# Optimization experiments

Measured on AMD Instinct MI355X. Metric: run time of the kernel, lower is better.

## Reference

```python
import jax, jax.numpy as jnp
import numpy as np

BETA = 0.01
NUM_EMBEDDINGS = 8192
EMBEDDING_DIM = 512


def setup_inputs() -> dict:
    key = jax.random.key(0)
    k1, k2 = jax.random.split(key)
    inputs = jax.random.normal(k1, (16, 2048, EMBEDDING_DIM), dtype=jnp.float32)
    # nn.Embedding weight init: uniform(-1/K, 1/K)
    lim = 1.0 / NUM_EMBEDDINGS
    codebook = jax.random.uniform(k2, (NUM_EMBEDDINGS, EMBEDDING_DIM),
                                  dtype=jnp.float32, minval=-lim, maxval=lim)
    return {"inputs": inputs, "codebook": codebook}


def reference(inputs, codebook):
    D = codebook.shape[1]
    x = inputs.reshape(-1, D)  # [N, D]
    distances = (jnp.sum(x * x, axis=1, keepdims=True)
                 + jnp.sum(codebook * codebook, axis=1)
                 - 2.0 * jnp.einsum('nd,kd->nk', x, codebook))
    encoding_indices = jnp.argmin(distances, axis=1)  # [N]
    quantized = codebook[encoding_indices].reshape(inputs.shape)
    sg = jax.lax.stop_gradient
    mse = lambda a, b: jnp.mean((a - b) ** 2)
    commitment_loss = mse(sg(quantized), inputs) + BETA * mse(quantized, sg(inputs))
    # straight-through estimator
    quantized_st = inputs + sg(quantized - inputs)
    return quantized_st, commitment_loss, encoding_indices
```

## Files before the change

kernel.cpp:

```cpp
#include <hip/hip_runtime.h>
#include <hip/hip_bf16.h>
#include <hip/hip_fp16.h>

typedef unsigned short ushortT;
typedef _Float16 half8 __attribute__((ext_vector_type(8)));
typedef float f32x4 __attribute__((ext_vector_type(4)));

#define N_ROWS   32768
#define DIM      512
#define K_CODES  8192
#define BETA     0.01f

#define LOSS_OFF 16777216
#define IDX_OFF  16777217

#define SC_XH_F      0
#define SC_EH_F      8388608
#define SC_GCODE_F   10485760
#define SC_GCNT_F    11010048
#define SC_FIXMIN_F  11042816
#define SC_FIXLIST_F 11108352

#define WS_XX_OFF     0
#define WS_IDX_OFF    32768
#define WS_PART_OFF   65536
#define WS_CNT_OFF    73728

#define FLT_BIG 3.402823466e+38f
#define W_ACC   0.08192f
#define GCAP    16

typedef __attribute__((address_space(1))) const unsigned int GUI;
typedef __attribute__((address_space(3))) unsigned int LUI;
__device__ __forceinline__ void gload16(const void* g, void* l) {
    __builtin_amdgcn_global_load_lds((GUI*)g, (LUI*)l, 16, 0, 0);
}

__global__ __launch_bounds__(256) void vq_prep(const float* __restrict__ x,
                                               const float* __restrict__ cb,
                                               ushortT* __restrict__ xh,
                                               ushortT* __restrict__ eh) {
    const size_t gid = (size_t)blockIdx.x * 256 + threadIdx.x;
    const size_t off8 = gid * 8;
    const float* src;
    ushortT* dst;
    float sc;
    if (off8 < 16777216UL) { src = x + off8; dst = xh + off8; sc = 1.0f; }
    else { size_t o = off8 - 16777216UL; src = cb + o; dst = eh + o; sc = 1024.0f; }
    float4 v0 = *reinterpret_cast<const float4*>(src);
    float4 v1 = *reinterpret_cast<const float4*>(src + 4);
    union { ushortT s[8]; uint4 v; } u;
    u.s[0] = __half_as_ushort(__float2half(v0.x * sc));
    u.s[1] = __half_as_ushort(__float2half(v0.y * sc));
    u.s[2] = __half_as_ushort(__float2half(v0.z * sc));
    u.s[3] = __half_as_ushort(__float2half(v0.w * sc));
    u.s[4] = __half_as_ushort(__float2half(v1.x * sc));
    u.s[5] = __half_as_ushort(__float2half(v1.y * sc));
    u.s[6] = __half_as_ushort(__float2half(v1.z * sc));
    u.s[7] = __half_as_ushort(__float2half(v1.w * sc));
    *reinterpret_cast<uint4*>(dst) = u.v;
}

__global__ __launch_bounds__(256) void vq_xx_kernel(const float* __restrict__ x,
                                                    float* __restrict__ xx) {
    __shared__ float l[4][512];
    const int wave = threadIdx.x >> 6;
    const int lane = threadIdx.x & 63;
    const int row = blockIdx.x * 4 + wave;
    const float* xr = x + (size_t)row * DIM;
#pragma unroll
    for (int i = 0; i < 2; ++i) {
        float4 v = *reinterpret_cast<const float4*>(xr + lane * 8 + i * 4);
        float4 q = make_float4(v.x * v.x, v.y * v.y, v.z * v.z, v.w * v.w);
        *reinterpret_cast<float4*>(&l[wave][lane * 8 + i * 4]) = q;
    }
    __syncthreads();
    if (lane == 0) {
        float B[4];
#pragma unroll
        for (int q = 0; q < 4; ++q) {
            const float* a = &l[wave][q * 128];
            float r0 = a[0], r1 = a[1], r2 = a[2], r3 = a[3];
            float r4 = a[4], r5 = a[5], r6 = a[6], r7 = a[7];
            for (int i = 8; i < 128; i += 8) {
                r0 += a[i + 0]; r1 += a[i + 1]; r2 += a[i + 2]; r3 += a[i + 3];
                r4 += a[i + 4]; r5 += a[i + 5]; r6 += a[i + 6]; r7 += a[i + 7];
            }
            B[q] = ((r0 + r1) + (r2 + r3)) + ((r4 + r5) + (r6 + r7));
        }
        xx[row] = (B[0] + B[1]) + (B[2] + B[3]);
    }
}

#define BM 128
#define BN 128
#define BKH 64
#define KHALF 4096
#define NSTEP 256
#define ABUF 8192

__global__ __launch_bounds__(512, 4) void vq_margmin(
    const ushortT* __restrict__ xh, const ushortT* __restrict__ eh,
    unsigned* __restrict__ gCode, unsigned* __restrict__ gCnt,
    int* __restrict__ fixcnt, int* __restrict__ fixlist) {
    __shared__ ushortT As[2][ABUF];
    __shared__ ushortT Bs[2][ABUF];
    float* v1L        = (float*)&As[0][0];
    float* rowThr     = (float*)&As[0][512];
    unsigned* candCnt = (unsigned*)&As[0][768];
    int* flagL        = (int*)&As[0][1024];
    ushortT* candList = &As[0][1280];

    const int t = threadIdx.x;
    const int l = t & 63;
    const int wid = t >> 6;
    const int wm = wid >> 1;
    const int wn = wid & 1;
    const int lr = l & 15;
    const int lg = l >> 4;
    const int rowBase = (blockIdx.x >> 1) * BM;
    const int kbase = (blockIdx.x & 1) * KHALF;

    const ushortT* aSrc0; const ushortT* aSrc1;
    const ushortT* bSrc0; const ushortT* bSrc1;
    int dOff0, dOff1;
    {
        int f0 = t, r0 = f0 >> 3, g0 = f0 & 7, gs0 = g0 ^ (r0 & 7);
        int f1 = t + 512, r1 = f1 >> 3, g1 = f1 & 7, gs1 = g1 ^ (r1 & 7);
        aSrc0 = xh + (size_t)(rowBase + r0) * DIM + gs0 * 8;
        aSrc1 = xh + (size_t)(rowBase + r1) * DIM + gs1 * 8;
        bSrc0 = eh + (size_t)(kbase + r0) * DIM + gs0 * 8;
        bSrc1 = eh + (size_t)(kbase + r1) * DIM + gs1 * 8;
        dOff0 = f0 * 8; dOff1 = f1 * 8;
    }
    int offA[2][2], offB[4][2];
#pragma unroll
    for (int kk = 0; kk < 2; ++kk) {
#pragma unroll
        for (int mf = 0; mf < 2; ++mf) {
            int row = wm * 32 + mf * 16 + lr;
            int pg = (kk * 4 + lg) ^ (row & 7);
            offA[mf][kk] = row * 128 + pg * 16;
        }
#pragma unroll
        for (int nf = 0; nf < 4; ++nf) {
            int col = wn * 64 + nf * 16 + lr;
            int pg = (kk * 4 + lg) ^ (col & 7);
            offB[nf][kk] = col * 128 + pg * 16;
        }
    }

    float v1[2][4], v2m[2][4], v3m[2][4];
    int i1[2][4], i2[2][4];
#pragma unroll
    for (int mf = 0; mf < 2; ++mf)
#pragma unroll
        for (int rr = 0; rr < 4; ++rr) {
            v1[mf][rr] = -FLT_BIG; v2m[mf][rr] = -FLT_BIG; v3m[mf][rr] = -FLT_BIG;
            i1[mf][rr] = 0; i2[mf][rr] = 0;
        }

    f32x4 acc[2][4];

#define STAGE(stp, b) do {                                                     \
    int kt_ = ((stp) & 7) * BKH;                                               \
    size_t bAdd_ = (size_t)((stp) >> 3) * BN * DIM + kt_;                      \
    gload16(aSrc0 + kt_, &As[b][dOff0]);                                       \
    gload16(aSrc1 + kt_, &As[b][dOff1]);                                       \
    gload16(bSrc0 + bAdd_, &Bs[b][dOff0]);                                     \
    gload16(bSrc1 + bAdd_, &Bs[b][dOff1]);                                     \
} while (0)

#define COMPUTE(CUR) do {                                                      \
    _Pragma("unroll")                                                          \
    for (int kk = 0; kk < 2; ++kk) {                                           \
        half8 a0 = *reinterpret_cast<const half8*>((const char*)&As[CUR][0] + offA[0][kk]); \
        half8 a1 = *reinterpret_cast<const half8*>((const char*)&As[CUR][0] + offA[1][kk]); \
        half8 b0 = *reinterpret_cast<const half8*>((const char*)&Bs[CUR][0] + offB[0][kk]); \
        half8 b1 = *reinterpret_cast<const half8*>((const char*)&Bs[CUR][0] + offB[1][kk]); \
        half8 b2 = *reinterpret_cast<const half8*>((const char*)&Bs[CUR][0] + offB[2][kk]); \
        half8 b3 = *reinterpret_cast<const half8*>((const char*)&Bs[CUR][0] + offB[3][kk]); \
        acc[0][0] = __builtin_amdgcn_mfma_f32_16x16x32_f16(a0, b0, acc[0][0], 0, 0, 0); \
        acc[0][1] = __builtin_amdgcn_mfma_f32_16x16x32_f16(a0, b1, acc[0][1], 0, 0, 0); \
        acc[0][2] = __builtin_amdgcn_mfma_f32_16x16x32_f16(a0, b2, acc[0][2], 0, 0, 0); \
        acc[0][3] = __builtin_amdgcn_mfma_f32_16x16x32_f16(a0, b3, acc[0][3], 0, 0, 0); \
        acc[1][0] = __builtin_amdgcn_mfma_f32_16x16x32_f16(a1, b0, acc[1][0], 0, 0, 0); \
        acc[1][1] = __builtin_amdgcn_mfma_f32_16x16x32_f16(a1, b1, acc[1][1], 0, 0, 0); \
        acc[1][2] = __builtin_amdgcn_mfma_f32_16x16x32_f16(a1, b2, acc[1][2], 0, 0, 0); \
        acc[1][3] = __builtin_amdgcn_mfma_f32_16x16x32_f16(a1, b3, acc[1][3], 0, 0, 0); \
    }                                                                          \
} while (0)

#define EPILOGUE(k0t_) do {                                                    \
    _Pragma("unroll")                                                          \
    for (int mf = 0; mf < 2; ++mf) {                                           \
        _Pragma("unroll")                                                      \
        for (int nf = 0; nf < 4; ++nf) {                                       \
            const int tag = ((k0t_) << 2) | nf;                                \
            _Pragma("unroll")                                                  \
            for (int rr = 0; rr < 4; ++rr) {                                   \
                float s = acc[mf][nf][rr];                                     \
                bool g1 = s > v1[mf][rr];                                      \
                bool g2 = s > v2m[mf][rr];                                     \
                bool g3 = s > v3m[mf][rr];                                     \
                v3m[mf][rr] = g2 ? v2m[mf][rr] : (g3 ? s : v3m[mf][rr]);       \
                i2[mf][rr]  = g1 ? i1[mf][rr]  : (g2 ? tag : i2[mf][rr]);      \
                v2m[mf][rr] = g1 ? v1[mf][rr]  : (g2 ? s : v2m[mf][rr]);       \
                i1[mf][rr]  = g1 ? tag : i1[mf][rr];                           \
                v1[mf][rr]  = g1 ? s   : v1[mf][rr];                           \
            }                                                                  \
        }                                                                      \
    }                                                                          \
} while (0)

    STAGE(0, 0);
    for (int sp = 0; sp < NSTEP; sp += 2) {
        if ((sp & 7) == 0) {
#pragma unroll
            for (int mf = 0; mf < 2; ++mf)
#pragma unroll
                for (int nf = 0; nf < 4; ++nf)
                    acc[mf][nf] = (f32x4){0.f, 0.f, 0.f, 0.f};
        }
        STAGE(sp + 1, 1);
        asm volatile("s_waitcnt vmcnt(4)" ::: "memory");
        __builtin_amdgcn_sched_barrier(0);
        __builtin_amdgcn_s_barrier();
        COMPUTE(0);
        __builtin_amdgcn_s_barrier();
        if (sp + 2 < NSTEP) {
            STAGE(sp + 2, 0);
            asm volatile("s_waitcnt vmcnt(4)" ::: "memory");
        } else {
            asm volatile("s_waitcnt vmcnt(0)" ::: "memory");
        }
        __builtin_amdgcn_sched_barrier(0);
        __builtin_amdgcn_s_barrier();
        COMPUTE(1);
        if ((sp & 7) == 6) EPILOGUE(sp >> 3);
        __builtin_amdgcn_s_barrier();
    }

    __syncthreads();
#pragma unroll
    for (int mf = 0; mf < 2; ++mf)
#pragma unroll
        for (int rr = 0; rr < 4; ++rr) {
            float v = v1[mf][rr];
            v = fmaxf(v, __shfl_xor(v, 1));
            v = fmaxf(v, __shfl_xor(v, 2));
            v = fmaxf(v, __shfl_xor(v, 4));
            v = fmaxf(v, __shfl_xor(v, 8));
            if (lr == 0) v1L[(wm * 32 + mf * 16 + lg * 4 + rr) * 2 + wn] = v;
        }
    __syncthreads();
    if (t < BM) {
        rowThr[t] = fmaxf(v1L[t * 2], v1L[t * 2 + 1]) - W_ACC;
        candCnt[t] = 0u;
        flagL[t] = 0;
    }
    __syncthreads();
#pragma unroll
    for (int mf = 0; mf < 2; ++mf)
#pragma unroll
        for (int rr = 0; rr < 4; ++rr) {
            const int row = wm * 32 + mf * 16 + lg * 4 + rr;
            const float thr = rowThr[row];
            if (v1[mf][rr] >= thr) {
                unsigned pos = atomicAdd(&candCnt[row], 1u);
                int tg = i1[mf][rr];
                int code = kbase + ((tg >> 2) << 7) + (wn << 6) + ((tg & 3) << 4) + lr;
                if (pos < GCAP) candList[row * GCAP + pos] = (ushortT)code;
                else flagL[row] = 1;
            }
            if (v2m[mf][rr] >= thr) {
                unsigned pos = atomicAdd(&candCnt[row], 1u);
                int tg = i2[mf][rr];
                int code = kbase + ((tg >> 2) << 7) + (wn << 6) + ((tg & 3) << 4) + lr;
                if (pos < GCAP) candList[row * GCAP + pos] = (ushortT)code;
                else flagL[row] = 1;
            }
            if (v3m[mf][rr] >= thr) flagL[row] = 1;
        }
    __syncthreads();
    if (t < BM) {
        const int grow = rowBase + t;
        unsigned cc = candCnt[t];
        bool ovf = (flagL[t] != 0) || (cc > GCAP);
        if (!ovf) {
            for (unsigned j = 0; j < cc; ++j) {
                unsigned pos = atomicAdd(&gCnt[grow], 1u);
                if (pos < GCAP) gCode[(size_t)grow * GCAP + pos] = candList[t * GCAP + j];
                else ovf = true;
            }
        }
        if (ovf) {
            int p = atomicAdd(fixcnt, 1);
            fixlist[p] = grow;
        }
    }
#undef STAGE
#undef COMPUTE
#undef EPILOGUE
}

__global__ __launch_bounds__(256) void vq_refine(
    const float* __restrict__ x, const float* __restrict__ cb,
    const float* __restrict__ xx, const unsigned* __restrict__ gCode,
    const unsigned* __restrict__ gCnt, float* __restrict__ outIdxF,
    int* __restrict__ idxI) {
    const int wave = threadIdx.x >> 6;
    const int lane = threadIdx.x & 63;
    const int row = blockIdx.x * 4 + wave;
    const unsigned cc = gCnt[row];
    if (cc == 0u || cc > GCAP) return;
    const float* xr = x + (size_t)row * DIM;
    float4 xa = *reinterpret_cast<const float4*>(xr + lane * 8);
    float4 xb = *reinterpret_cast<const float4*>(xr + lane * 8 + 4);
    const float xxrow = xx[row];
    float best = FLT_BIG;
    int bi = 0x7fffffff;
    for (unsigned c = 0; c < cc; ++c) {
        int code = (int)gCode[(size_t)row * GCAP + c];
        const float* er = cb + (size_t)code * DIM;
        float4 ea = *reinterpret_cast<const float4*>(er + lane * 8);
        float4 eb = *reinterpret_cast<const float4*>(er + lane * 8 + 4);
        double p = (double)xa.x * ea.x + (double)xa.y * ea.y
                 + (double)xa.z * ea.z + (double)xa.w * ea.w
                 + (double)xb.x * eb.x + (double)xb.y * eb.y
                 + (double)xb.z * eb.z + (double)xb.w * eb.w;
#pragma unroll
        for (int off = 1; off < 64; off <<= 1) p += __shfl_xor(p, off);
        float sc = xxrow - (float)(2.0 * p);
        if (sc < best || (sc == best && code < bi)) { best = sc; bi = code; }
    }
    if (lane == 0) { idxI[row] = bi; outIdxF[row] = (float)bi; }
}

__global__ __launch_bounds__(256) void vq_fixup_scan(
    const float* __restrict__ x, const float* __restrict__ cb,
    const float* __restrict__ xx, const int* __restrict__ cnt,
    const int* __restrict__ list, unsigned long long* __restrict__ fixmin) {
    const int nflag = *cnt;
    if (nflag == 0) return;
    const int gw = (blockIdx.x * 256 + threadIdx.x) >> 6;
    const int lane = threadIdx.x & 63;
    const int nwaves = gridDim.x * 4;
    const int totalUnits = nflag * 128;
    for (int u = gw; u < totalUnits; u += nwaves) {
        const int row = list[u >> 7];
        const int kb = (u & 127) * 64;
        const float* xr = x + (size_t)row * DIM;
        float4 xa = *reinterpret_cast<const float4*>(xr + lane * 8);
        float4 xb = *reinterpret_cast<const float4*>(xr + lane * 8 + 4);
        const float xxrow = xx[row];
        unsigned long long best = ~0ULL;
        for (int k = kb; k < kb + 64; ++k) {
            const float* er = cb + (size_t)k * DIM;
            float4 ea = *reinterpret_cast<const float4*>(er + lane * 8);
            float4 eb = *reinterpret_cast<const float4*>(er + lane * 8 + 4);
            double p = (double)xa.x * ea.x + (double)xa.y * ea.y
                     + (double)xa.z * ea.z + (double)xa.w * ea.w
                     + (double)xb.x * eb.x + (double)xb.y * eb.y
                     + (double)xb.z * eb.z + (double)xb.w * eb.w;
#pragma unroll
            for (int off = 1; off < 64; off <<= 1) p += __shfl_xor(p, off);
            float sc = xxrow - (float)(2.0 * p);
            unsigned long long key =
                ((unsigned long long)__float_as_uint(sc) << 32) | (unsigned)k;
            best = (key < best) ? key : best;
        }
        if (lane == 0) atomicMin(&fixmin[row], best);
    }
}

__global__ __launch_bounds__(256) void vq_fixup_write(
    const int* __restrict__ cnt, const int* __restrict__ list,
    const unsigned long long* __restrict__ fixmin,
    float* __restrict__ outIdxF, int* __restrict__ idxI) {
    const int i = blockIdx.x * 256 + threadIdx.x;
    if (i >= *cnt) return;
    const int row = list[i];
    const int code = (int)(unsigned)(fixmin[row] & 0xFFFFFFFFULL);
    idxI[row] = code;
    outIdxF[row] = (float)code;
}

__global__ __launch_bounds__(256) void vq_gather_kernel(
    const float* __restrict__ x, const float* __restrict__ cb,
    const int* __restrict__ idxI, float* __restrict__ outQ,
    float* __restrict__ partial) {
    const int wave = threadIdx.x >> 6;
    const int lane = threadIdx.x & 63;
    const int row = blockIdx.x * 4 + wave;
    const int code = idxI[row];
    const float* xr = x + (size_t)row * DIM;
    const float* er = cb + (size_t)code * DIM;
    float* qr = outQ + (size_t)row * DIM;
    float s = 0.f;
#pragma unroll
    for (int i = 0; i < 2; ++i) {
        int d = lane * 8 + i * 4;
        float4 xv = *reinterpret_cast<const float4*>(xr + d);
        float4 ev = *reinterpret_cast<const float4*>(er + d);
        float4 dv = make_float4(ev.x - xv.x, ev.y - xv.y, ev.z - xv.z, ev.w - xv.w);
        *reinterpret_cast<float4*>(qr + d) = ev;
        s += dv.x * dv.x + dv.y * dv.y + dv.z * dv.z + dv.w * dv.w;
    }
#pragma unroll
    for (int off = 32; off > 0; off >>= 1) s += __shfl_xor(s, off);
    __shared__ float ws4[4];
    if (lane == 0) ws4[wave] = s;
    __syncthreads();
    if (threadIdx.x == 0)
        partial[blockIdx.x] = (ws4[0] + ws4[1]) + (ws4[2] + ws4[3]);
}

__global__ __launch_bounds__(256) void vq_loss_kernel(const float* __restrict__ partial,
                                                      float* __restrict__ outLoss) {
    float s = 0.f;
    for (int i = threadIdx.x; i < 8192; i += 256) s += partial[i];
    __shared__ float sm[256];
    sm[threadIdx.x] = s;
    __syncthreads();
    for (int off = 128; off > 0; off >>= 1) {
        if (threadIdx.x < off) sm[threadIdx.x] += sm[threadIdx.x + off];
        __syncthreads();
    }
    if (threadIdx.x == 0)
        outLoss[0] = sm[0] * (1.0f + BETA) / 16777216.0f;
}

extern "C" void kernel_launch(void* const* d_in, const int* in_sizes, int n_in,
                              void* d_out, int out_size, void* d_ws, size_t ws_size,
                              hipStream_t stream) {
    const float* x = (const float*)d_in[0];
    const float* cb = (const float*)d_in[1];
    float* out = (float*)d_out;

    ushortT* xh = (ushortT*)out;
    ushortT* eh = (ushortT*)(out + SC_EH_F);
    unsigned* gCode = (unsigned*)(out + SC_GCODE_F);
    unsigned* gCnt = (unsigned*)(out + SC_GCNT_F);
    unsigned long long* fixmin = (unsigned long long*)(out + SC_FIXMIN_F);
    int* fixlist = (int*)(out + SC_FIXLIST_F);

    float* xx = (float*)d_ws + WS_XX_OFF;
    int* idxI = (int*)d_ws + WS_IDX_OFF;
    float* partial = (float*)d_ws + WS_PART_OFF;
    int* fixcnt = (int*)d_ws + WS_CNT_OFF;

    hipMemsetAsync(fixcnt, 0, sizeof(int), stream);
    hipMemsetAsync(gCnt, 0, N_ROWS * sizeof(unsigned), stream);
    hipMemsetAsync(fixmin, 0xFF, N_ROWS * sizeof(unsigned long long), stream);
    hipLaunchKernelGGL(vq_prep, dim3(10240), dim3(256), 0, stream, x, cb, xh, eh);
    hipLaunchKernelGGL(vq_xx_kernel, dim3(N_ROWS / 4), dim3(256), 0, stream, x, xx);
    hipLaunchKernelGGL(vq_margmin, dim3((N_ROWS / BM) * 2), dim3(512), 0, stream,
                       xh, eh, gCode, gCnt, fixcnt, fixlist);
    hipLaunchKernelGGL(vq_refine, dim3(N_ROWS / 4), dim3(256), 0, stream,
                       x, cb, xx, gCode, gCnt, out + IDX_OFF, idxI);
    hipLaunchKernelGGL(vq_fixup_scan, dim3(2048), dim3(256), 0, stream,
                       x, cb, xx, fixcnt, fixlist, fixmin);
    hipLaunchKernelGGL(vq_fixup_write, dim3(256), dim3(256), 0, stream,
                       fixcnt, fixlist, fixmin, out + IDX_OFF, idxI);
    hipLaunchKernelGGL(vq_gather_kernel, dim3(N_ROWS / 4), dim3(256), 0, stream,
                       x, cb, idxI, out, partial);
    hipLaunchKernelGGL(vq_loss_kernel, dim3(1), dim3(256), 0, stream,
                       partial, out + LOSS_OFF);
}
```

Measured before the change: 553.9 us.

## Enlarge margmin row tile to 256, split codebook in quarters, single-buffer LDS

The candidate-search GEMM moves from 128-row tiles over half the codebook to 256-row tiles over a quarter of it. Each wave now computes a 64x64 output tile, and the codebook operand becomes the MFMA A side so each lane tracks its own row in the running top-2 state. This removes the intra-wave shuffle reduction over 16 lanes and raises arithmetic intensity per LDS load. The double-buffered, explicitly scheduled prefetch pipeline is replaced by a single buffer guarded by two __syncthreads per step, so global loads no longer overlap compute. The larger accumulator array also adds register pressure.

```diff
diff --git a/kernel.cpp b/kernel.cpp
--- a/kernel.cpp
+++ b/kernel.cpp
@@ -92,167 +92,149 @@
     }
 }
 
-#define BM 128
+#define BM 256
 #define BN 128
 #define BKH 64
-#define KHALF 4096
-#define NSTEP 256
-#define ABUF 8192
+#define KHALF 2048
+#define NSTEP 128
 
 __global__ __launch_bounds__(512, 4) void vq_margmin(
     const ushortT* __restrict__ xh, const ushortT* __restrict__ eh,
     unsigned* __restrict__ gCode, unsigned* __restrict__ gCnt,
     int* __restrict__ fixcnt, int* __restrict__ fixlist) {
-    __shared__ ushortT As[2][ABUF];
-    __shared__ ushortT Bs[2][ABUF];
-    float* v1L        = (float*)&As[0][0];
-    float* rowThr     = (float*)&As[0][512];
-    unsigned* candCnt = (unsigned*)&As[0][768];
-    int* flagL        = (int*)&As[0][1024];
-    ushortT* candList = &As[0][1280];
+    __shared__ ushortT Rs[BM * BKH];
+    __shared__ ushortT Cs[BN * BKH];
+    float* v1L        = (float*)&Rs[0];
+    float* rowThr     = (float*)&Rs[1024];
+    unsigned* candCnt = (unsigned*)&Rs[1536];
+    int* flagL        = (int*)&Rs[2048];
+    ushortT* candList = &Rs[2560];
 
     const int t = threadIdx.x;
     const int l = t & 63;
     const int wid = t >> 6;
-    const int wm = wid >> 1;
-    const int wn = wid & 1;
+    const int wr = wid >> 1;
+    const int wc = wid & 1;
     const int lr = l & 15;
     const int lg = l >> 4;
-    const int rowBase = (blockIdx.x >> 1) * BM;
-    const int kbase = (blockIdx.x & 1) * KHALF;
-
-    const ushortT* aSrc0; const ushortT* aSrc1;
-    const ushortT* bSrc0; const ushortT* bSrc1;
-    int dOff0, dOff1;
+    const int rowBase = (blockIdx.x >> 2) * BM;
+    const int kbase = (blockIdx.x & 3) * KHALF;
+
+    const ushortT* rSrc0; const ushortT* rSrc1; const ushortT* rSrc2; const ushortT* rSrc3;
+    const ushortT* cSrc0; const ushortT* cSrc1;
+    int rD0, rD1, rD2, rD3, cD0, cD1;
     {
-        int f0 = t, r0 = f0 >> 3, g0 = f0 & 7, gs0 = g0 ^ (r0 & 7);
-        int f1 = t + 512, r1 = f1 >> 3, g1 = f1 & 7, gs1 = g1 ^ (r1 & 7);
-        aSrc0 = xh + (size_t)(rowBase + r0) * DIM + gs0 * 8;
-        aSrc1 = xh + (size_t)(rowBase + r1) * DIM + gs1 * 8;
-        bSrc0 = eh + (size_t)(kbase + r0) * DIM + gs0 * 8;
-        bSrc1 = eh + (size_t)(kbase + r1) * DIM + gs1 * 8;
-        dOff0 = f0 * 8; dOff1 = f1 * 8;
-    }
-    int offA[2][2], offB[4][2];
-#pragma unroll
-    for (int kk = 0; kk < 2; ++kk) {
-#pragma unroll
-        for (int mf = 0; mf < 2; ++mf) {
-            int row = wm * 32 + mf * 16 + lr;
-            int pg = (kk * 4 + lg) ^ (row & 7);
-            offA[mf][kk] = row * 128 + pg * 16;
-        }
-#pragma unroll
-        for (int nf = 0; nf < 4; ++nf) {
-            int col = wn * 64 + nf * 16 + lr;
-            int pg = (kk * 4 + lg) ^ (col & 7);
-            offB[nf][kk] = col * 128 + pg * 16;
-        }
-    }
-
-    float v1[2][4], v2m[2][4], v3m[2][4];
-    int i1[2][4], i2[2][4];
-#pragma unroll
-    for (int mf = 0; mf < 2; ++mf)
-#pragma unroll
-        for (int rr = 0; rr < 4; ++rr) {
-            v1[mf][rr] = -FLT_BIG; v2m[mf][rr] = -FLT_BIG; v3m[mf][rr] = -FLT_BIG;
-            i1[mf][rr] = 0; i2[mf][rr] = 0;
-        }
-
-    f32x4 acc[2][4];
-
-#define STAGE(stp, b) do {                                                     \
+        int f0 = t,        r0 = f0 >> 3, gs0 = (f0 & 7) ^ (r0 & 7);
+        int f1 = t + 512,  r1 = f1 >> 3, gs1 = (f1 & 7) ^ (r1 & 7);
+        int f2 = t + 1024, r2 = f2 >> 3, gs2 = (f2 & 7) ^ (r2 & 7);
+        int f3 = t + 1536, r3 = f3 >> 3, gs3 = (f3 & 7) ^ (r3 & 7);
+        rSrc0 = xh + (size_t)(rowBase + r0) * DIM + gs0 * 8;
+        rSrc1 = xh + (size_t)(rowBase + r1) * DIM + gs1 * 8;
+        rSrc2 = xh + (size_t)(rowBase + r2) * DIM + gs2 * 8;
+        rSrc3 = xh + (size_t)(rowBase + r3) * DIM + gs3 * 8;
+        rD0 = f0 * 8; rD1 = f1 * 8; rD2 = f2 * 8; rD3 = f3 * 8;
+        cSrc0 = eh + (size_t)(kbase + r0) * DIM + gs0 * 8;
+        cSrc1 = eh + (size_t)(kbase + r1) * DIM + gs1 * 8;
+        cD0 = f0 * 8; cD1 = f1 * 8;
+    }
+    int cB0 = (wc * 64 + 0 * 16 + lr) * 64, cB1 = (wc * 64 + 1 * 16 + lr) * 64;
+    int cB2 = (wc * 64 + 2 * 16 + lr) * 64, cB3 = (wc * 64 + 3 * 16 + lr) * 64;
+    int rB0 = (wr * 64 + 0 * 16 + lr) * 64, rB1 = (wr * 64 + 1 * 16 + lr) * 64;
+    int rB2 = (wr * 64 + 2 * 16 + lr) * 64, rB3 = (wr * 64 + 3 * 16 + lr) * 64;
+
+    float v1[4], v2m[4], v3m[4];
+    int i1[4], i2[4];
+#pragma unroll
+    for (int nf = 0; nf < 4; ++nf) {
+        v1[nf] = -FLT_BIG; v2m[nf] = -FLT_BIG; v3m[nf] = -FLT_BIG;
+        i1[nf] = 0; i2[nf] = 0;
+    }
+
+    f32x4 acc[4][4];
+
+#define STAGE(stp) do {                                                        \
     int kt_ = ((stp) & 7) * BKH;                                               \
-    size_t bAdd_ = (size_t)((stp) >> 3) * BN * DIM + kt_;                      \
-    gload16(aSrc0 + kt_, &As[b][dOff0]);                                       \
-    gload16(aSrc1 + kt_, &As[b][dOff1]);                                       \
-    gload16(bSrc0 + bAdd_, &Bs[b][dOff0]);                                     \
-    gload16(bSrc1 + bAdd_, &Bs[b][dOff1]);                                     \
+    size_t cAdd_ = (size_t)((stp) >> 3) * BN * DIM + kt_;                      \
+    gload16(rSrc0 + kt_, &Rs[rD0]);                                            \
+    gload16(rSrc1 + kt_, &Rs[rD1]);                                            \
+    gload16(rSrc2 + kt_, &Rs[rD2]);                                            \
+    gload16(rSrc3 + kt_, &Rs[rD3]);                                            \
+    gload16(cSrc0 + cAdd_, &Cs[cD0]);                                          \
+    gload16(cSrc1 + cAdd_, &Cs[cD1]);                                          \
 } while (0)
 
-#define COMPUTE(CUR) do {                                                      \
-    _Pragma("unroll")                                                          \
-    for (int kk = 0; kk < 2; ++kk) {                                           \
-        half8 a0 = *reinterpret_cast<const half8*>((const char*)&As[CUR][0] + offA[0][kk]); \
-        half8 a1 = *reinterpret_cast<const half8*>((const char*)&As[CUR][0] + offA[1][kk]); \
-        half8 b0 = *reinterpret_cast<const half8*>((const char*)&Bs[CUR][0] + offB[0][kk]); \
-        half8 b1 = *reinterpret_cast<const half8*>((const char*)&Bs[CUR][0] + offB[1][kk]); \
-        half8 b2 = *reinterpret_cast<const half8*>((const char*)&Bs[CUR][0] + offB[2][kk]); \
-        half8 b3 = *reinterpret_cast<const half8*>((const char*)&Bs[CUR][0] + offB[3][kk]); \
-        acc[0][0] = __builtin_amdgcn_mfma_f32_16x16x32_f16(a0, b0, acc[0][0], 0, 0, 0); \
-        acc[0][1] = __builtin_amdgcn_mfma_f32_16x16x32_f16(a0, b1, acc[0][1], 0, 0, 0); \
-        acc[0][2] = __builtin_amdgcn_mfma_f32_16x16x32_f16(a0, b2, acc[0][2], 0, 0, 0); \
-        acc[0][3] = __builtin_amdgcn_mfma_f32_16x16x32_f16(a0, b3, acc[0][3], 0, 0, 0); \
-        acc[1][0] = __builtin_amdgcn_mfma_f32_16x16x32_f16(a1, b0, acc[1][0], 0, 0, 0); \
-        acc[1][1] = __builtin_amdgcn_mfma_f32_16x16x32_f16(a1, b1, acc[1][1], 0, 0, 0); \
-        acc[1][2] = __builtin_amdgcn_mfma_f32_16x16x32_f16(a1, b2, acc[1][2], 0, 0, 0); \
-        acc[1][3] = __builtin_amdgcn_mfma_f32_16x16x32_f16(a1, b3, acc[1][3], 0, 0, 0); \
-    }                                                                          \
-} while (0)
-
-#define EPILOGUE(k0t_) do {                                                    \
-    _Pragma("unroll")                                                          \
-    for (int mf = 0; mf < 2; ++mf) {                                           \
-        _Pragma("unroll")                                                      \
-        for (int nf = 0; nf < 4; ++nf) {                                       \
-            const int tag = ((k0t_) << 2) | nf;                                \
-            _Pragma("unroll")                                                  \
-            for (int rr = 0; rr < 4; ++rr) {                                   \
-                float s = acc[mf][nf][rr];                                     \
-                bool g1 = s > v1[mf][rr];                                      \
-                bool g2 = s > v2m[mf][rr];                                     \
-                bool g3 = s > v3m[mf][rr];                                     \
-                v3m[mf][rr] = g2 ? v2m[mf][rr] : (g3 ? s : v3m[mf][rr]);       \
-                i2[mf][rr]  = g1 ? i1[mf][rr]  : (g2 ? tag : i2[mf][rr]);      \
-                v2m[mf][rr] = g1 ? v1[mf][rr]  : (g2 ? s : v2m[mf][rr]);       \
-                i1[mf][rr]  = g1 ? tag : i1[mf][rr];                           \
-                v1[mf][rr]  = g1 ? s   : v1[mf][rr];                           \
-            }                                                                  \
-        }                                                                      \
-    }                                                                          \
-} while (0)
-
-    STAGE(0, 0);
-    for (int sp = 0; sp < NSTEP; sp += 2) {
-        if ((sp & 7) == 0) {
-#pragma unroll
-            for (int mf = 0; mf < 2; ++mf)
+    for (int step = 0; step < NSTEP; ++step) {
+        if ((step & 7) == 0) {
+#pragma unroll
+            for (int mf = 0; mf < 4; ++mf)
 #pragma unroll
                 for (int nf = 0; nf < 4; ++nf)
                     acc[mf][nf] = (f32x4){0.f, 0.f, 0.f, 0.f};
         }
-        STAGE(sp + 1, 1);
-        asm volatile("s_waitcnt vmcnt(4)" ::: "memory");
-        __builtin_amdgcn_sched_barrier(0);
-        __builtin_amdgcn_s_barrier();
-        COMPUTE(0);
-        __builtin_amdgcn_s_barrier();
-        if (sp + 2 < NSTEP) {
-            STAGE(sp + 2, 0);
-            asm volatile("s_waitcnt vmcnt(4)" ::: "memory");
-        } else {
-            asm volatile("s_waitcnt vmcnt(0)" ::: "memory");
-        }
-        __builtin_amdgcn_sched_barrier(0);
-        __builtin_amdgcn_s_barrier();
-        COMPUTE(1);
-        if ((sp & 7) == 6) EPILOGUE(sp >> 3);
-        __builtin_amdgcn_s_barrier();
-    }
-
-    __syncthreads();
-#pragma unroll
-    for (int mf = 0; mf < 2; ++mf)
-#pragma unroll
-        for (int rr = 0; rr < 4; ++rr) {
-            float v = v1[mf][rr];
-            v = fmaxf(v, __shfl_xor(v, 1));
-            v = fmaxf(v, __shfl_xor(v, 2));
-            v = fmaxf(v, __shfl_xor(v, 4));
-            v = fmaxf(v, __shfl_xor(v, 8));
-            if (lr == 0) v1L[(wm * 32 + mf * 16 + lg * 4 + rr) * 2 + wn] = v;
-        }
+        __syncthreads();
+        STAGE(step);
+        __syncthreads();
+#pragma unroll
+        for (int kk = 0; kk < 2; ++kk) {
+            const int sl = ((kk << 2) + lg) ^ (lr & 7);
+            half8 a0 = *reinterpret_cast<const half8*>(&Cs[cB0 + sl * 8]);
+            half8 a1 = *reinterpret_cast<const half8*>(&Cs[cB1 + sl * 8]);
+            half8 a2 = *reinterpret_cast<const half8*>(&Cs[cB2 + sl * 8]);
+            half8 a3 = *reinterpret_cast<const half8*>(&Cs[cB3 + sl * 8]);
+            half8 b0 = *reinterpret_cast<const half8*>(&Rs[rB0 + sl * 8]);
+            half8 b1 = *reinterpret_cast<const half8*>(&Rs[rB1 + sl * 8]);
+            half8 b2 = *reinterpret_cast<const half8*>(&Rs[rB2 + sl * 8]);
+            half8 b3 = *reinterpret_cast<const half8*>(&Rs[rB3 + sl * 8]);
+            acc[0][0] = __builtin_amdgcn_mfma_f32_16x16x32_f16(a0, b0, acc[0][0], 0, 0, 0);
+            acc[0][1] = __builtin_amdgcn_mfma_f32_16x16x32_f16(a0, b1, acc[0][1], 0, 0, 0);
+            acc[0][2] = __builtin_amdgcn_mfma_f32_16x16x32_f16(a0, b2, acc[0][2], 0, 0, 0);
+            acc[0][3] = __builtin_amdgcn_mfma_f32_16x16x32_f16(a0, b3, acc[0][3], 0, 0, 0);
+            acc[1][0] = __builtin_amdgcn_mfma_f32_16x16x32_f16(a1, b0, acc[1][0], 0, 0, 0);
+            acc[1][1] = __builtin_amdgcn_mfma_f32_16x16x32_f16(a1, b1, acc[1][1], 0, 0, 0);
+            acc[1][2] = __builtin_amdgcn_mfma_f32_16x16x32_f16(a1, b2, acc[1][2], 0, 0, 0);
+            acc[1][3] = __builtin_amdgcn_mfma_f32_16x16x32_f16(a1, b3, acc[1][3], 0, 0, 0);
+            acc[2][0] = __builtin_amdgcn_mfma_f32_16x16x32_f16(a2, b0, acc[2][0], 0, 0, 0);
+            acc[2][1] = __builtin_amdgcn_mfma_f32_16x16x32_f16(a2, b1, acc[2][1], 0, 0, 0);
+            acc[2][2] = __builtin_amdgcn_mfma_f32_16x16x32_f16(a2, b2, acc[2][2], 0, 0, 0);
+            acc[2][3] = __builtin_amdgcn_mfma_f32_16x16x32_f16(a2, b3, acc[2][3], 0, 0, 0);
+            acc[3][0] = __builtin_amdgcn_mfma_f32_16x16x32_f16(a3, b0, acc[3][0], 0, 0, 0);
+            acc[3][1] = __builtin_amdgcn_mfma_f32_16x16x32_f16(a3, b1, acc[3][1], 0, 0, 0);
+            acc[3][2] = __builtin_amdgcn_mfma_f32_16x16x32_f16(a3, b2, acc[3][2], 0, 0, 0);
+            acc[3][3] = __builtin_amdgcn_mfma_f32_16x16x32_f16(a3, b3, acc[3][3], 0, 0, 0);
+        }
+        if ((step & 7) == 7) {
+            const int k0t = step >> 3;
+#pragma unroll
+            for (int nf = 0; nf < 4; ++nf) {
+#pragma unroll
+                for (int mf = 0; mf < 4; ++mf) {
+                    const int tagB = (k0t << 4) | (mf << 2);
+#pragma unroll
+                    for (int rr = 0; rr < 4; ++rr) {
+                        float s = acc[mf][nf][rr];
+                        bool g1 = s > v1[nf];
+                        bool g2 = s > v2m[nf];
+                        bool g3 = s > v3m[nf];
+                        v3m[nf] = g2 ? v2m[nf] : (g3 ? s : v3m[nf]);
+                        i2[nf]  = g1 ? i1[nf]  : (g2 ? (tagB | rr) : i2[nf]);
+                        v2m[nf] = g1 ? v1[nf]  : (g2 ? s : v2m[nf]);
+                        i1[nf]  = g1 ? (tagB | rr) : i1[nf];
+                        v1[nf]  = g1 ? s : v1[nf];
+                    }
+                }
+            }
+        }
+    }
+#undef STAGE
+
+    __syncthreads();
+#pragma unroll
+    for (int nf = 0; nf < 4; ++nf) {
+        float v = v1[nf];
+        v = fmaxf(v, __shfl_xor(v, 16));
+        v = fmaxf(v, __shfl_xor(v, 32));
+        if (l < 16) v1L[(wr * 64 + nf * 16 + l) * 2 + wc] = v;
+    }
     __syncthreads();
     if (t < BM) {
         rowThr[t] = fmaxf(v1L[t * 2], v1L[t * 2 + 1]) - W_ACC;
@@ -261,27 +243,25 @@
     }
     __syncthreads();
 #pragma unroll
-    for (int mf = 0; mf < 2; ++mf)
-#pragma unroll
-        for (int rr = 0; rr < 4; ++rr) {
-            const int row = wm * 32 + mf * 16 + lg * 4 + rr;
-            const float thr = rowThr[row];
-            if (v1[mf][rr] >= thr) {
-                unsigned pos = atomicAdd(&candCnt[row], 1u);
-                int tg = i1[mf][rr];
-                int code = kbase + ((tg >> 2) << 7) + (wn << 6) + ((tg & 3) << 4) + lr;
-                if (pos < GCAP) candList[row * GCAP + pos] = (ushortT)code;
-                else flagL[row] = 1;
-            }
-            if (v2m[mf][rr] >= thr) {
-                unsigned pos = atomicAdd(&candCnt[row], 1u);
-                int tg = i2[mf][rr];
-                int code = kbase + ((tg >> 2) << 7) + (wn << 6) + ((tg & 3) << 4) + lr;
-                if (pos < GCAP) candList[row * GCAP + pos] = (ushortT)code;
-                else flagL[row] = 1;
-            }
-            if (v3m[mf][rr] >= thr) flagL[row] = 1;
-        }
+    for (int nf = 0; nf < 4; ++nf) {
+        const int row = wr * 64 + nf * 16 + lr;
+        const float thr = rowThr[row];
+        if (v1[nf] >= thr) {
+            unsigned pos = atomicAdd(&candCnt[row], 1u);
+            int tg = i1[nf];
+            int code = kbase + ((tg >> 4) << 7) + wc * 64 + (((tg >> 2) & 3) << 4) + lg * 4 + (tg & 3);
+            if (pos < GCAP) candList[row * GCAP + pos] = (ushortT)code;
+            else flagL[row] = 1;
+        }
+        if (v2m[nf] >= thr) {
+            unsigned pos = atomicAdd(&candCnt[row], 1u);
+            int tg = i2[nf];
+            int code = kbase + ((tg >> 4) << 7) + wc * 64 + (((tg >> 2) & 3) << 4) + lg * 4 + (tg & 3);
+            if (pos < GCAP) candList[row * GCAP + pos] = (ushortT)code;
+            else flagL[row] = 1;
+        }
+        if (v3m[nf] >= thr) flagL[row] = 1;
+    }
     __syncthreads();
     if (t < BM) {
         const int grow = rowBase + t;
@@ -299,9 +279,6 @@
             fixlist[p] = grow;
         }
     }
-#undef STAGE
-#undef COMPUTE
-#undef EPILOGUE
 }
 
 __global__ __launch_bounds__(256) void vq_refine(
@@ -455,7 +432,7 @@
     hipMemsetAsync(fixmin, 0xFF, N_ROWS * sizeof(unsigned long long), stream);
     hipLaunchKernelGGL(vq_prep, dim3(10240), dim3(256), 0, stream, x, cb, xh, eh);
     hipLaunchKernelGGL(vq_xx_kernel, dim3(N_ROWS / 4), dim3(256), 0, stream, x, xx);
-    hipLaunchKernelGGL(vq_margmin, dim3((N_ROWS / BM) * 2), dim3(512), 0, stream,
+    hipLaunchKernelGGL(vq_margmin, dim3((N_ROWS / BM) * 4), dim3(512), 0, stream,
                        xh, eh, gCode, gCnt, fixcnt, fixlist);
     hipLaunchKernelGGL(vq_refine, dim3(N_ROWS / 4), dim3(256), 0, stream,
                        x, cb, xx, gCode, gCnt, out + IDX_OFF, idxI);
```

After: 582.6 us. 5.2% more time.
